# Kernel tuning notes

Hardware: AMD Instinct MI355X
Metric: run time of the kernel (lower is better)

## Reference

```python
import jax, jax.numpy as jnp
import numpy as np

N = 50000        # nodes
E = 800000       # edges (avg degree 16)
HID = 256        # hidden_size
HEADS = 8        # num_heads
HD = HID // HEADS  # head_dim = 32


def setup_inputs() -> dict:
    key = jax.random.key(0)
    ks = jax.random.split(key, 10)
    h = jax.random.normal(ks[0], (N, HID), dtype=jnp.float32)
    val = jax.random.uniform(ks[1], (E,), dtype=jnp.float32)
    Wq = jax.random.normal(ks[2], (HID, HID), dtype=jnp.float32) * 0.02
    Wk = jax.random.normal(ks[3], (HID, HID), dtype=jnp.float32) * 0.02
    Wv = jax.random.normal(ks[4], (HID, HID), dtype=jnp.float32) * 0.02
    bq = jnp.zeros((HID,), dtype=jnp.float32)
    bk = jnp.zeros((HID,), dtype=jnp.float32)
    bv = jnp.zeros((HID,), dtype=jnp.float32)
    # CSR rows expanded to per-edge row ids (sorted, like row_ptr expansion)
    edge_rows = jnp.sort(jax.random.randint(ks[5], (E,), 0, N, dtype=jnp.int32))
    col_ind = jax.random.randint(ks[6], (E,), 0, N, dtype=jnp.int32)
    return {"h": h, "val": val, "Wq": Wq, "bq": bq, "Wk": Wk, "bk": bk,
            "Wv": Wv, "bv": bv, "edge_rows": edge_rows, "col_ind": col_ind}


def reference(h, val, Wq, bq, Wk, bk, Wv, bv, edge_rows, col_ind):
    scaling = HD ** (-0.5)
    # projections; reshape splits hidden as (head_dim, heads) with heads fastest,
    # exactly as in the torch module: reshape(N, head_dim, num_heads)
    q = ((h @ Wq + bq).reshape(N, HD, HEADS)) * scaling
    k = (h @ Wk + bk).reshape(N, HD, HEADS)
    v = (h @ Wv + bv).reshape(N, HD, HEADS)

    # SDDMM restricted to edges: score[e, head] = <q[row_e], k[col_e]> * A.val[e]
    score = jnp.einsum('edh,edh->eh', q[edge_rows], k[col_ind]) * val[:, None]  # [E, HEADS]

    # per-destination-row softmax over incident edges (stable, segment ops)
    m = jax.ops.segment_max(score, edge_rows, num_segments=N)        # [N, HEADS]
    m = jnp.where(jnp.isfinite(m), m, jnp.zeros_like(m))             # empty rows
    e = jnp.exp(score - m[edge_rows])                                # [E, HEADS]
    denom = jax.ops.segment_sum(e, edge_rows, num_segments=N)        # [N, HEADS]
    attn = e / denom[edge_rows]

    # SpMM: out[i] = sum over edges (i, j) of attn * v[j]
    contrib = attn[:, None, :] * v[col_ind]                          # [E, HD, HEADS]
    out = jax.ops.segment_sum(contrib, edge_rows, num_segments=N)    # [N, HD, HEADS]
    return out.reshape(N, -1)                                        # [N, HID]
```

## Files before the change

### kernel.cpp

```cpp
#include <hip/hip_runtime.h>
#include <hip/hip_bf16.h>
#include <math.h>

static constexpr int kN   = 50000;
static constexpr int kE   = 800000;
static constexpr int kHID = 256;
static constexpr int kHD  = 32;

typedef short bf16x8 __attribute__((ext_vector_type(8)));
typedef float f32x4  __attribute__((ext_vector_type(4)));
typedef float f32x2  __attribute__((ext_vector_type(2)));
typedef unsigned short us8 __attribute__((ext_vector_type(8)));
typedef unsigned int u32x4 __attribute__((ext_vector_type(4)));
typedef int i32x2 __attribute__((ext_vector_type(2)));
typedef int i32x4 __attribute__((ext_vector_type(4)));

__device__ __forceinline__ float b2f(unsigned short u) {
  union { unsigned v; float f; } c; c.v = ((unsigned)u) << 16; return c.f;
}

__device__ __forceinline__ unsigned short f2bu(float f) {
  __hip_bfloat16 b = __float2bfloat16(f);
  union { __hip_bfloat16 b; unsigned short u; } c; c.b = b; return c.u;
}

__device__ __forceinline__ f32x2 bf2up(unsigned u) {
  union { unsigned v; float f; } lo, hi;
  lo.v = u << 16; hi.v = u & 0xffff0000u;
  return f32x2{lo.f, hi.f};
}

__device__ __forceinline__ float quad_add_xor1(float s) {
  union { float f; int i; } a, b;
  a.f = s;
  b.i = __builtin_amdgcn_mov_dpp(a.i, 0xB1, 0xF, 0xF, true);
  return s + b.f;
}
__device__ __forceinline__ float quad_add_xor2(float s) {
  union { float f; int i; } a, b;
  a.f = s;
  b.i = __builtin_amdgcn_mov_dpp(a.i, 0x4E, 0xF, 0xF, true);
  return s + b.f;
}

__device__ __forceinline__ void load_lds16(const void* g, void* l) {
  __builtin_amdgcn_global_load_lds(
      (const __attribute__((address_space(1))) unsigned int*)(unsigned long long)(uintptr_t)g,
      (__attribute__((address_space(3))) unsigned int*)(unsigned int)(uintptr_t)l,
      16, 0, 0);
}

__global__ void prep_all_kernel(
    const float* __restrict__ h, __hip_bfloat16* __restrict__ Ah,
    const float* __restrict__ Wq, const float* __restrict__ bq,
    const float* __restrict__ Wk, const float* __restrict__ bk,
    const float* __restrict__ Wv, const float* __restrict__ bv,
    __hip_bfloat16* __restrict__ Bt, float* __restrict__ biasP,
    const int* __restrict__ er, int* __restrict__ rp,
    const int* __restrict__ ci, const float* __restrict__ vl,
    i32x2* __restrict__ cv) {
  int b = blockIdx.x;
  if (b < 6250) {
    int idx = b * 256 + threadIdx.x;
    const f32x4* hp = (const f32x4*)(h + (size_t)idx * 8);
    f32x4 a = hp[0], c = hp[1];
    us8 o;
    o[0] = f2bu(a[0]); o[1] = f2bu(a[1]); o[2] = f2bu(a[2]); o[3] = f2bu(a[3]);
    o[4] = f2bu(c[0]); o[5] = f2bu(c[1]); o[6] = f2bu(c[2]); o[7] = f2bu(c[3]);
    *(us8*)(Ah + (size_t)idx * 8) = o;
    return;
  }
  b -= 6250;
  if (b < 768) {
    const int n  = b;
    const int kk = threadIdx.x;
    const int g  = n >> 8;
    const int cc = n & 255;
    const int c  = ((cc & 31) << 3) + (cc >> 5);
    const float scale = (g == 0) ? 0.17677669529663689f : 1.0f;
    const float* W = (g == 0) ? Wq : ((g == 1) ? Wk : Wv);
    Bt[n * 256 + kk] = __float2bfloat16(W[kk * 256 + c] * scale);
    if (kk == 0) {
      const float* bb = (g == 0) ? bq : ((g == 1) ? bk : bv);
      biasP[n] = bb[c] * scale;
    }
    return;
  }
  b -= 768;
  if (b < 196) {
    int i = b * 256 + threadIdx.x;
    if (i > kN) return;
    int lo = 0, hi = kE;
    while (lo < hi) {
      int mid = (lo + hi) >> 1;
      if (er[mid] < i) lo = mid + 1; else hi = mid;
    }
    rp[i] = lo;
    return;
  }
  b -= 196;
  {
    const int e4 = (b * 256 + threadIdx.x) * 4;
    if (e4 < kE) {
      i32x4 c = *(const i32x4*)(ci + e4);
      f32x4 w = *(const f32x4*)(vl + e4);
      i32x4 o0 = {c[0], __float_as_int(w[0]), c[1], __float_as_int(w[1])};
      i32x4 o1 = {c[2], __float_as_int(w[2]), c[3], __float_as_int(w[3])};
      *(i32x4*)(cv + e4)     = o0;
      *(i32x4*)(cv + e4 + 2) = o1;
    }
  }
}

__global__ __launch_bounds__(256) void gemm_qkv_kernel(
    const __hip_bfloat16* __restrict__ Ah,
    const __hip_bfloat16* __restrict__ Bt, const float* __restrict__ biasP,
    __hip_bfloat16* __restrict__ qb, __hip_bfloat16* __restrict__ kvb) {
  __shared__ __align__(16) char smemRaw[65536];
  short* smemC = (short*)smemRaw;

  const int L   = blockIdx.x;
  const int xcd = L & 7;
  const int t_  = L >> 3;
  const int nt  = t_ % 6;
  const int mg  = t_ / 6;
  const int mt  = mg * 8 + xcd;
  if (mt >= 391) return;
  const int colBase = nt * 128;
  const int rowBase = mt * 128;

  const int tid  = threadIdx.x;
  const int wave = tid >> 6;
  const int lane = tid & 63;
  const int wm = wave & 1;
  const int wn = wave >> 1;

  f32x4 acc[4][4];
#pragma unroll
  for (int i = 0; i < 4; ++i)
#pragma unroll
    for (int j = 0; j < 4; ++j) acc[i][j] = f32x4{0.f, 0.f, 0.f, 0.f};

#define STAGE(BUF, K0)                                                      \
  {                                                                         \
    char* dA = smemRaw + (BUF) * 32768;                                     \
    char* dB = dA + 16384;                                                  \
    _Pragma("unroll")                                                       \
    for (int j = 0; j < 4; ++j) {                                           \
      int s = (wave * 4 + j) * 64 + lane;                                   \
      int r = s >> 3, cp = s & 7;                                           \
      int c = cp ^ (r & 7);                                                 \
      int grow = rowBase + r;                                               \
      grow = grow < kN ? grow : kN - 1;                                     \
      load_lds16((const char*)Ah + (size_t)grow * 512 + (K0) * 2 + c * 16,  \
                 dA + (wave * 4 + j) * 1024);                               \
      load_lds16((const char*)Bt + (size_t)(colBase + r) * 512 + (K0) * 2 + c * 16, \
                 dB + (wave * 4 + j) * 1024);                               \
    }                                                                       \
  }

  STAGE(0, 0);
  __syncthreads();

  const int rq = lane & 15, qd = lane >> 4;
#pragma unroll
  for (int t = 0; t < 4; ++t) {
    if (t < 3) STAGE((t + 1) & 1, (t + 1) * 64);
    const short* sA = (const short*)(smemRaw + (t & 1) * 32768);
    const short* sB = sA + 8192;
#pragma unroll
    for (int ks = 0; ks < 2; ++ks) {
      bf16x8 af[4], bfr[4];
#pragma unroll
      for (int mi = 0; mi < 4; ++mi) {
        int r = wm * 64 + mi * 16 + rq;
        int c = (ks * 4 + qd) ^ (r & 7);
        af[mi] = *(const bf16x8*)&sA[r * 64 + c * 8];
      }
#pragma unroll
      for (int nj = 0; nj < 4; ++nj) {
        int r = wn * 64 + nj * 16 + rq;
        int c = (ks * 4 + qd) ^ (r & 7);
        bfr[nj] = *(const bf16x8*)&sB[r * 64 + c * 8];
      }
#pragma unroll
      for (int mi = 0; mi < 4; ++mi)
#pragma unroll
        for (int nj = 0; nj < 4; ++nj)
          acc[mi][nj] = __builtin_amdgcn_mfma_f32_16x16x32_bf16(
              af[mi], bfr[nj], acc[mi][nj], 0, 0, 0);
    }
    __syncthreads();
  }
#undef STAGE

#pragma unroll
  for (int nj = 0; nj < 4; ++nj) {
    const int cl = wn * 64 + nj * 16 + (lane & 15);
    const float bb = biasP[colBase + cl];
#pragma unroll
    for (int mi = 0; mi < 4; ++mi) {
      const int rl = wm * 64 + mi * 16 + (lane >> 4) * 4;
#pragma unroll
      for (int reg = 0; reg < 4; ++reg) {
        smemC[(rl + reg) * 136 + cl] = (short)f2bu(acc[mi][nj][reg] + bb);
      }
    }
  }
  __syncthreads();

  const int g = colBase >> 8;
#pragma unroll
  for (int it = 0; it < 8; ++it) {
    const int r   = it * 16 + (tid >> 4);
    const int c16 = tid & 15;
    const int row = rowBase + r;
    if (row < kN) {
      bf16x8 vls = *(const bf16x8*)&smemC[r * 136 + c16 * 8];
      const int cc = (colBase & 255) + c16 * 8;
      __hip_bfloat16* dst =
          (g == 0) ? (qb + (size_t)row * 256 + cc)
                   : (kvb + (size_t)row * 512 + (g == 2 ? 256 : 0) + cc);
      *(bf16x8*)dst = vls;
    }
  }
}

__global__ __launch_bounds__(128) void edge_attn_kernel(
    const __hip_bfloat16* __restrict__ qb, const __hip_bfloat16* __restrict__ kvb,
    const int* __restrict__ row_ptr, const i32x2* __restrict__ cvp,
    float* __restrict__ out) {
  const int wave = threadIdx.x >> 6;
  const int lane = threadIdx.x & 63;
  const int half = lane >> 5;
  const int sl   = lane & 31;
  const int row = blockIdx.x * 2 + wave;
  if (row >= kN) return;

  const int e0 = row_ptr[row];
  const int e1 = row_ptr[row + 1];

  const us8 qu = *(const us8*)(qb + (size_t)row * 256 + sl * 8);
  f32x2 qf2[4];
#pragma unroll
  for (int j = 0; j < 4; ++j)
    qf2[j] = f32x2{b2f(qu[2 * j]) * 1.4426950408889634f,
                   b2f(qu[2 * j + 1]) * 1.4426950408889634f};

  float denom = 0.f;
  f32x2 acc2[4];
#pragma unroll
  for (int j = 0; j < 4; ++j) acc2[j] = f32x2{0.f, 0.f};

  if (e0 < e1) {
    const char* kvbL = (const char*)kvb + sl * 16;
    const int elast = e1 - 1;

    u32x4 kS[4], vS[4];
    float wS[4];
    i32x2 cvA[4], cvB[4];

    i32x2 c0[4];
#pragma unroll
    for (int j = 0; j < 4; ++j) {
      const int ea = min(e0 + 2 * j + half, elast);
      c0[j] = cvp[ea];
    }
#pragma unroll
    for (int j = 0; j < 4; ++j) {
      const int eb = min(e0 + 8 + 2 * j + half, elast);
      cvA[j] = cvp[eb];
    }
#pragma unroll
    for (int j = 0; j < 4; ++j) {
      const int ec = min(e0 + 16 + 2 * j + half, elast);
      cvB[j] = cvp[ec];
    }
#pragma unroll
    for (int j = 0; j < 4; ++j) {
      const size_t off = (size_t)c0[j][0] * 1024;
      kS[j] = *(const u32x4*)(kvbL + off);
      vS[j] = *(const u32x4*)(kvbL + off + 512);
      wS[j] = __int_as_float(c0[j][1]);
    }

#define ATTN_GROUP(EB, CB)                                                \
    _Pragma("unroll")                                                     \
    for (int j = 0; j < 4; ++j) {                                         \
      const u32x4 kc = kS[j], vc = vS[j];                                 \
      const float wc = wS[j];                                             \
      {                                                                   \
        const size_t off = (size_t)CB[j][0] * 1024;                       \
        kS[j] = *(const u32x4*)(kvbL + off);                              \
        vS[j] = *(const u32x4*)(kvbL + off + 512);                        \
        wS[j] = __int_as_float(CB[j][1]);                                 \
      }                                                                   \
      {                                                                   \
        const int en = min((EB) + 24 + 2 * j + half, elast);              \
        CB[j] = cvp[en];                                                  \
      }                                                                   \
      f32x2 s2 = qf2[0] * bf2up(kc[0]);                                   \
      s2 += qf2[1] * bf2up(kc[1]);                                        \
      s2 += qf2[2] * bf2up(kc[2]);                                        \
      s2 += qf2[3] * bf2up(kc[3]);                                        \
      float s = s2[0] + s2[1];                                            \
      s = quad_add_xor1(s);                                               \
      s = quad_add_xor2(s);                \
      s *= wc;                                                            \
      float p = exp2f(s);                                                 \
      p = (((EB) + 2 * j + half) < e1) ? p : 0.f;                         \
      denom += p;                                                         \
      const f32x2 p2 = {p, p};                                            \
      acc2[0] += p2 * bf2up(vc[0]);                                       \
      acc2[1] += p2 * bf2up(vc[1]);                                       \
      acc2[2] += p2 * bf2up(vc[2]);                                       \
      acc2[3] += p2 * bf2up(vc[3]);                                       \
    }

    int e = e0;
    for (;;) {
      ATTN_GROUP(e, cvA);
      e += 8; if (e >= e1) break;
      ATTN_GROUP(e, cvB);
      e += 8; if (e >= e1) break;
    }
#undef ATTN_GROUP
  }

  float accs[8];
#pragma unroll
  for (int j = 0; j < 8; ++j) {
    float a = (j & 1) ? acc2[j >> 1][1] : acc2[j >> 1][0];
    accs[j] = a + __shfl_xor(a, 32);
  }
  denom += __shfl_xor(denom, 32);

  const float inv = (denom > 0.f) ? (1.0f / denom) : 0.f;
  const int h = sl >> 2;
  const int dbase = (sl & 3) * 8 + half * 4;
  float* o = out + (size_t)row * 256 + h;
#pragma unroll
  for (int jj = 0; jj < 4; ++jj)
    o[(dbase + jj) * 8] = accs[half * 4 + jj] * inv;
}

extern "C" void kernel_launch(void* const* d_in, const int* in_sizes, int n_in,
                              void* d_out, int out_size, void* d_ws, size_t ws_size,
                              hipStream_t stream) {
  const float* h   = (const float*)d_in[0];
  const float* val = (const float*)d_in[1];
  const float* Wq  = (const float*)d_in[2];
  const float* bq  = (const float*)d_in[3];
  const float* Wk  = (const float*)d_in[4];
  const float* bk  = (const float*)d_in[5];
  const float* Wv  = (const float*)d_in[6];
  const float* bv  = (const float*)d_in[7];
  const int* edge_rows = (const int*)d_in[8];
  const int* col_ind   = (const int*)d_in[9];
  float* out = (float*)d_out;

  char* ws = (char*)d_ws;
  __hip_bfloat16* Ah  = (__hip_bfloat16*)ws;                 ws += (size_t)kN * 256 * 2;
  __hip_bfloat16* Bt  = (__hip_bfloat16*)ws;                 ws += (size_t)768 * 256 * 2;
  float*          biasP = (float*)ws;                        ws += 768 * 4;
  __hip_bfloat16* qb  = (__hip_bfloat16*)ws;                 ws += (size_t)kN * 256 * 2;
  __hip_bfloat16* kvb = (__hip_bfloat16*)ws;                 ws += (size_t)kN * 512 * 2;
  int* row_ptr = (int*)ws;                                   ws += ((size_t)(kN + 1) * 4 + 127) & ~127ull;
  i32x2* cv = (i32x2*)ws;

  prep_all_kernel<<<6250 + 768 + 196 + 782, 256, 0, stream>>>(
      h, Ah, Wq, bq, Wk, bk, Wv, bv, Bt, biasP,
      edge_rows, row_ptr, col_ind, val, cv);

  gemm_qkv_kernel<<<8 * 6 * 49, 256, 0, stream>>>(Ah, Bt, biasP, qb, kvb);

  edge_attn_kernel<<<(kN + 1) / 2, 128, 0, stream>>>(qb, kvb, row_ptr, cv, out);
}
```

Before: 265.7 us.

## Process two rows per wave and prefetch next row's edges during current row

Result: no change. 268.0 us (+0.9%).

```diff
diff --git a/kernel.cpp b/kernel.cpp
--- a/kernel.cpp
+++ b/kernel.cpp
@@ -234,48 +234,38 @@
   const int lane = threadIdx.x & 63;
   const int half = lane >> 5;
   const int sl   = lane & 31;
-  const int row = blockIdx.x * 2 + wave;
-  if (row >= kN) return;
-
-  const int e0 = row_ptr[row];
-  const int e1 = row_ptr[row + 1];
-
-  const us8 qu = *(const us8*)(qb + (size_t)row * 256 + sl * 8);
-  f32x2 qf2[4];
-#pragma unroll
-  for (int j = 0; j < 4; ++j)
-    qf2[j] = f32x2{b2f(qu[2 * j]) * 1.4426950408889634f,
-                   b2f(qu[2 * j + 1]) * 1.4426950408889634f};
-
-  float denom = 0.f;
-  f32x2 acc2[4];
-#pragma unroll
-  for (int j = 0; j < 4; ++j) acc2[j] = f32x2{0.f, 0.f};
-
-  if (e0 < e1) {
-    const char* kvbL = (const char*)kvb + sl * 16;
-    const int elast = e1 - 1;
-
-    u32x4 kS[4], vS[4];
-    float wS[4];
-    i32x2 cvA[4], cvB[4];
-
+  const int r0 = blockIdx.x * 4 + wave * 2;
+  if (r0 >= kN) return;
+  const int r1 = r0 + 1;
+  const bool haveR1 = (r1 < kN);
+
+  const char* kvbL = (const char*)kvb + sl * 16;
+
+  const int e00 = row_ptr[r0];
+  const int e01 = row_ptr[r0 + 1];
+  const int eB1 = haveR1 ? row_ptr[r0 + 2] : e01;
+
+  const us8 qu0 = *(const us8*)(qb + (size_t)r0 * 256 + sl * 8);
+
+  u32x4 kS[4], vS[4]; float wS[4];
+  i32x2 cvA[4], cvB[4];
+  i32x2 c0N[4];
+
+  if (haveR1 && e01 < eB1) {
+    const int elB = eB1 - 1;
+#pragma unroll
+    for (int j = 0; j < 4; ++j) c0N[j] = cvp[min(e01 + 2 * j + half, elB)];
+  }
+
+  if (e00 < e01) {
+    const int elA = e01 - 1;
     i32x2 c0[4];
 #pragma unroll
-    for (int j = 0; j < 4; ++j) {
-      const int ea = min(e0 + 2 * j + half, elast);
-      c0[j] = cvp[ea];
-    }
-#pragma unroll
-    for (int j = 0; j < 4; ++j) {
-      const int eb = min(e0 + 8 + 2 * j + half, elast);
-      cvA[j] = cvp[eb];
-    }
-#pragma unroll
-    for (int j = 0; j < 4; ++j) {
-      const int ec = min(e0 + 16 + 2 * j + half, elast);
-      cvB[j] = cvp[ec];
-    }
+    for (int j = 0; j < 4; ++j) c0[j] = cvp[min(e00 + 2 * j + half, elA)];
+#pragma unroll
+    for (int j = 0; j < 4; ++j) cvA[j] = cvp[min(e00 + 8 + 2 * j + half, elA)];
+#pragma unroll
+    for (int j = 0; j < 4; ++j) cvB[j] = cvp[min(e00 + 16 + 2 * j + half, elA)];
 #pragma unroll
     for (int j = 0; j < 4; ++j) {
       const size_t off = (size_t)c0[j][0] * 1024;
@@ -283,6 +273,18 @@
       vS[j] = *(const u32x4*)(kvbL + off + 512);
       wS[j] = __int_as_float(c0[j][1]);
     }
+  }
+
+  float qf2a[8];
+#pragma unroll
+  for (int j = 0; j < 8; ++j) qf2a[j] = b2f(qu0[j]) * 1.4426950408889634f;
+
+  float denom = 0.f;
+  f32x2 acc2[4];
+#pragma unroll
+  for (int j = 0; j < 4; ++j) acc2[j] = f32x2{0.f, 0.f};
+
+  int e0, e1, elast;
 
 #define ATTN_GROUP(EB, CB)                                                \
     _Pragma("unroll")                                                     \
@@ -299,10 +301,10 @@
         const int en = min((EB) + 24 + 2 * j + half, elast);              \
         CB[j] = cvp[en];                                                  \
       }                                                                   \
-      f32x2 s2 = qf2[0] * bf2up(kc[0]);                                   \
-      s2 += qf2[1] * bf2up(kc[1]);                                        \
-      s2 += qf2[2] * bf2up(kc[2]);                                        \
-      s2 += qf2[3] * bf2up(kc[3]);                                        \
+      f32x2 s2 = f32x2{qf2a[0], qf2a[1]} * bf2up(kc[0]);                  \
+      s2 += f32x2{qf2a[2], qf2a[3]} * bf2up(kc[1]);                       \
+      s2 += f32x2{qf2a[4], qf2a[5]} * bf2up(kc[2]);                       \
+      s2 += f32x2{qf2a[6], qf2a[7]} * bf2up(kc[3]);                       \
       float s = s2[0] + s2[1];                                            \
       s = quad_add_xor1(s);                                               \
       s = quad_add_xor2(s);                \
@@ -317,31 +319,76 @@
       acc2[3] += p2 * bf2up(vc[3]);                                       \
     }
 
-    int e = e0;
-    for (;;) {
-      ATTN_GROUP(e, cvA);
-      e += 8; if (e >= e1) break;
-      ATTN_GROUP(e, cvB);
-      e += 8; if (e >= e1) break;
-    }
+#define ROW_LOOP                                                          \
+    {                                                                     \
+      int e = e0;                                                         \
+      for (;;) {                                                          \
+        ATTN_GROUP(e, cvA);                                               \
+        e += 8; if (e >= e1) break;                                       \
+        ATTN_GROUP(e, cvB);                                               \
+        e += 8; if (e >= e1) break;                                       \
+      }                                                                   \
+    }
+
+#define ROW_EPILOGUE(R)                                                   \
+    {                                                                     \
+      float accs[8];                                                      \
+      _Pragma("unroll")                                                   \
+      for (int j = 0; j < 8; ++j) {                                       \
+        float a = (j & 1) ? acc2[j >> 1][1] : acc2[j >> 1][0];            \
+        accs[j] = a + __shfl_xor(a, 32);                                  \
+      }                                                                   \
+      float dn = denom + __shfl_xor(denom, 32);                           \
+      const float inv = (dn > 0.f) ? (1.0f / dn) : 0.f;                   \
+      const int hh = sl >> 2;                                             \
+      const int dbase = (sl & 3) * 8 + half * 4;                          \
+      float* o = out + (size_t)(R) * 256 + hh;                            \
+      _Pragma("unroll")                                                   \
+      for (int jj = 0; jj < 4; ++jj)                                      \
+        o[(dbase + jj) * 8] = accs[half * 4 + jj] * inv;                  \
+    }
+
+  if (e00 < e01) {
+    e0 = e00; e1 = e01; elast = e01 - 1;
+    ROW_LOOP;
+  }
+
+  us8 qu1;
+  if (haveR1) {
+    qu1 = *(const us8*)(qb + (size_t)r1 * 256 + sl * 8);
+    if (e01 < eB1) {
+      const int elB = eB1 - 1;
+#pragma unroll
+      for (int j = 0; j < 4; ++j) {
+        const size_t off = (size_t)c0N[j][0] * 1024;
+        kS[j] = *(const u32x4*)(kvbL + off);
+        vS[j] = *(const u32x4*)(kvbL + off + 512);
+        wS[j] = __int_as_float(c0N[j][1]);
+      }
+#pragma unroll
+      for (int j = 0; j < 4; ++j) cvA[j] = cvp[min(e01 + 8 + 2 * j + half, elB)];
+#pragma unroll
+      for (int j = 0; j < 4; ++j) cvB[j] = cvp[min(e01 + 16 + 2 * j + half, elB)];
+    }
+  }
+
+  ROW_EPILOGUE(r0);
+
+  if (haveR1) {
+#pragma unroll
+    for (int j = 0; j < 8; ++j) qf2a[j] = b2f(qu1[j]) * 1.4426950408889634f;
+    denom = 0.f;
+#pragma unroll
+    for (int j = 0; j < 4; ++j) acc2[j] = f32x2{0.f, 0.f};
+    if (e01 < eB1) {
+      e0 = e01; e1 = eB1; elast = eB1 - 1;
+      ROW_LOOP;
+    }
+    ROW_EPILOGUE(r1);
+  }
 #undef ATTN_GROUP
-  }
-
-  float accs[8];
-#pragma unroll
-  for (int j = 0; j < 8; ++j) {
-    float a = (j & 1) ? acc2[j >> 1][1] : acc2[j >> 1][0];
-    accs[j] = a + __shfl_xor(a, 32);
-  }
-  denom += __shfl_xor(denom, 32);
-
-  const float inv = (denom > 0.f) ? (1.0f / denom) : 0.f;
-  const int h = sl >> 2;
-  const int dbase = (sl & 3) * 8 + half * 4;
-  float* o = out + (size_t)row * 256 + h;
-#pragma unroll
-  for (int jj = 0; jj < 4; ++jj)
-    o[(dbase + jj) * 8] = accs[half * 4 + jj] * inv;
+#undef ROW_LOOP
+#undef ROW_EPILOGUE
 }
 
 extern "C" void kernel_launch(void* const* d_in, const int* in_sizes, int n_in,
@@ -374,5 +421,5 @@
 
   gemm_qkv_kernel<<<8 * 6 * 49, 256, 0, stream>>>(Ah, Bt, biasP, qb, kvb);
 
-  edge_attn_kernel<<<(kN + 1) / 2, 128, 0, stream>>>(qb, kvb, row_ptr, cv, out);
-}
+  edge_attn_kernel<<<(kN + 3) / 4, 128, 0, stream>>>(qb, kvb, row_ptr, cv, out);
+}
```
